# Performance work log

Hardware: AMD Instinct MI355X
Metric: run time of the kernel (lower is better)

Reference implementation:

```python
import jax, jax.numpy as jnp
import numpy as np

N_NODES = 100000
N_EDGES = 400000
IN_FEATS = 64
H_FEATS = 128
INTER = 128
NUM_CLASSES = 64


def setup_inputs() -> dict:
    key = jax.random.key(0)
    ks = jax.random.split(key, 32)
    inp = {}
    inp['gate_type'] = jax.random.randint(ks[0], (N_NODES,), 0, IN_FEATS)
    inp['src'] = jax.random.randint(ks[1], (N_EDGES,), 0, N_NODES)
    inp['dst'] = jax.random.randint(ks[2], (N_EDGES,), 0, N_NODES)
    inp['src_idx'] = jax.random.uniform(ks[3], (N_EDGES,), dtype=jnp.float32)
    inp['dst_idx'] = jax.random.uniform(ks[4], (N_EDGES,), dtype=jnp.float32)
    inp['rev'] = jax.random.uniform(ks[5], (N_EDGES,), dtype=jnp.float32)
    inp['emb'] = jax.random.normal(ks[6], (IN_FEATS, IN_FEATS), dtype=jnp.float32) * 0.05
    dims = [(IN_FEATS, H_FEATS), (H_FEATS, H_FEATS), (H_FEATS, H_FEATS), (H_FEATS, H_FEATS), (H_FEATS, NUM_CLASSES)]
    k = 7
    for i, (fi, fo) in enumerate(dims, 1):
        # xavier-normal-like scaling
        inp[f'w1_{i}'] = jax.random.normal(ks[k], (INTER, fi + 3), dtype=jnp.float32) * np.float32(np.sqrt(2.0 / (fi + 3 + INTER))); k += 1
        inp[f'w2_{i}'] = jax.random.normal(ks[k], (fo, fi + INTER), dtype=jnp.float32) * np.float32(np.sqrt(2.0 / (fi + INTER + fo))); k += 1
        inp[f'b2_{i}'] = jnp.zeros((fo,), dtype=jnp.float32); k += 1
    return inp


def _qconv(h, src, dst, w_edge, W1, W2, b2):
    # message: concat src node feats with edge feats -> [E, d+3]
    m = jnp.concatenate([h[src], w_edge], axis=1)
    # linear1 (no bias) + leaky_relu (torch default slope 0.01)
    tmp = jax.nn.leaky_relu(m @ W1.T, negative_slope=0.01)  # [E, inter]
    # mean-reduce per destination node (isolated nodes -> zeros, matching DGL)
    s = jax.ops.segment_sum(tmp, dst, num_segments=h.shape[0])
    cnt = jax.ops.segment_sum(jnp.ones((dst.shape[0],), tmp.dtype), dst, num_segments=h.shape[0])
    h_N = s / jnp.maximum(cnt, 1.0)[:, None]
    # linear2 on [h, h_N]
    return jnp.concatenate([h, h_N], axis=1) @ W2.T + b2


def reference(gate_type, src, dst, src_idx, dst_idx, rev, emb,
              w1_1, w2_1, b2_1, w1_2, w2_2, b2_2, w1_3, w2_3, b2_3,
              w1_4, w2_4, b2_4, w1_5, w2_5, b2_5):
    h = emb[gate_type]  # [N, in_feats]
    w_edge = jnp.stack([src_idx, dst_idx, rev], axis=1)  # [E, 3]
    layers = [(w1_1, w2_1, b2_1), (w1_2, w2_2, b2_2), (w1_3, w2_3, b2_3),
              (w1_4, w2_4, b2_4), (w1_5, w2_5, b2_5)]
    for i, (W1, W2, b2) in enumerate(layers):
        h = _qconv(h, src, dst, w_edge, W1, W2, b2)
        if i < 4:
            h = jax.nn.relu(h)
    return h
```

## Files before the change

### kernel.cpp

```cpp
#include <hip/hip_runtime.h>
#include <hip/hip_fp16.h>

typedef __attribute__((ext_vector_type(8))) short short8;
typedef __attribute__((ext_vector_type(4))) float f32x4;
typedef unsigned short u16;

__device__ __forceinline__ u16 f2bf(float f) {
    unsigned u = __float_as_uint(f);
    unsigned r = ((u >> 16) & 1) + 0x7FFFu;
    return (u16)((u + r) >> 16);
}

__device__ __forceinline__ unsigned pk_fma(unsigned a, unsigned b, unsigned c) {
    unsigned d;
    asm("v_pk_fma_f16 %0, %1, %2, %3" : "=v"(d) : "v"(a), "v"(b), "v"(c));
    return d;
}
__device__ __forceinline__ unsigned pk_mul(unsigned a, unsigned b) {
    unsigned d;
    asm("v_pk_mul_f16 %0, %1, %2" : "=v"(d) : "v"(a), "v"(b));
    return d;
}
__device__ __forceinline__ unsigned pk_max(unsigned a, unsigned b) {
    unsigned d;
    asm("v_pk_max_f16 %0, %1, %2" : "=v"(d) : "v"(a), "v"(b));
    return d;
}


__global__ void k_count(const int* __restrict__ dst, int* __restrict__ cnt, int E) {
    int i = blockIdx.x * 256 + threadIdx.x;
    if (i < E) atomicAdd(&cnt[dst[i]], 1);
}

__global__ void k_scan1(const int* __restrict__ cnt, int* __restrict__ partial, int N) {
    __shared__ int sm[256];
    int idx = blockIdx.x * 256 + threadIdx.x;
    sm[threadIdx.x] = (idx < N) ? cnt[idx] : 0;
    __syncthreads();
    for (int s = 128; s > 0; s >>= 1) {
        if (threadIdx.x < s) sm[threadIdx.x] += sm[threadIdx.x + s];
        __syncthreads();
    }
    if (threadIdx.x == 0) partial[blockIdx.x] = sm[0];
}

__global__ void k_scan2(int* __restrict__ partial, int nb) {
    __shared__ int sm[512];
    int t = threadIdx.x;
    sm[t] = (t < nb) ? partial[t] : 0;
    __syncthreads();
    for (int off = 1; off < 512; off <<= 1) {
        int v = (t >= off) ? sm[t - off] : 0;
        __syncthreads();
        sm[t] += v;
        __syncthreads();
    }
    if (t < nb) partial[t] = (t == 0) ? 0 : sm[t - 1];
}

__global__ void k_scan3(const int* __restrict__ cnt, const int* __restrict__ partial,
                        int* __restrict__ row_off, int* __restrict__ cursor,
                        float* __restrict__ invdeg, int N, int E) {
    __shared__ int sm[256];
    int idx = blockIdx.x * 256 + threadIdx.x;
    int v = (idx < N) ? cnt[idx] : 0;
    sm[threadIdx.x] = v;
    __syncthreads();
    for (int off = 1; off < 256; off <<= 1) {
        int u = (threadIdx.x >= off) ? sm[threadIdx.x - off] : 0;
        __syncthreads();
        sm[threadIdx.x] += u;
        __syncthreads();
    }
    if (idx < N) {
        int excl = partial[blockIdx.x] + sm[threadIdx.x] - v;
        row_off[idx] = excl;
        cursor[idx] = excl;
        invdeg[idx] = 1.0f / (float)((v > 1) ? v : 1);
    }
    if (idx == 0) row_off[N] = E;
}

__global__ void k_scatter(const int* __restrict__ dst, const int* __restrict__ src,
                          const float* __restrict__ sidx, const float* __restrict__ didx,
                          const float* __restrict__ rev,
                          int* __restrict__ cursor, int4* __restrict__ payload, int E) {
    int i = blockIdx.x * 256 + threadIdx.x;
    if (i < E) {
        int p = atomicAdd(&cursor[dst[i]], 1);
        unsigned hs = (unsigned)__half_as_ushort(__float2half_rn(sidx[i]));
        unsigned hd = (unsigned)__half_as_ushort(__float2half_rn(didx[i]));
        unsigned hr = (unsigned)__half_as_ushort(__float2half_rn(rev[i]));
        int4 v;
        v.x = src[i];
        v.y = (int)(hs * 0x10001u);
        v.z = (int)(hd * 0x10001u);
        v.w = (int)(hr * 0x10001u);
        payload[p] = v;
    }
}


__global__ void k_emb(const int* __restrict__ gt, const float* __restrict__ emb,
                      u16* __restrict__ h0, int N) {
    int i = blockIdx.x * 256 + threadIdx.x;
    if (i < N * 64) {
        int n = i >> 6, f = i & 63;
        h0[i] = f2bf(emb[(gt[n] << 6) | f]);
    }
}


struct WDesc {
    const float* src[10];
    u16* dst[10];
    int scols[10];
    int dcols[10];
    int n[10];
};

__global__ void k_wconv(WDesc d) {
    int seg = blockIdx.y;
    int idx = blockIdx.x * 256 + threadIdx.x;
    if (idx < d.n[seg]) {
        int dc = d.dcols[seg];
        int r = idx / dc, c = idx % dc;
        d.dst[seg][idx] = f2bf(d.src[seg][r * d.scols[seg] + c]);
    }
}

struct EDesc {
    const float* src[5];
    unsigned* dst[5];
    int ldw[5];
    int fi[5];
};

__global__ void k_wedge(EDesc d) {
    int l = blockIdx.x;
    int i = threadIdx.x;
    if (i < 192) {
        int c = i >> 6, j = i & 63;
        float a = d.src[l][(size_t)(2 * j) * d.ldw[l] + d.fi[l] + c];
        float b = d.src[l][(size_t)(2 * j + 1) * d.ldw[l] + d.fi[l] + c];
        unsigned lo = (unsigned)__half_as_ushort(__float2half_rn(a));
        unsigned hi = (unsigned)__half_as_ushort(__float2half_rn(b));
        d.dst[l][(c << 6) + j] = lo | (hi << 16);
    }
}


__global__ __launch_bounds__(256)
void k_edge(int N,
            const int* __restrict__ row_off, const int4* __restrict__ payload,
            const u16* __restrict__ g,
            const unsigned* __restrict__ W1h,
            const float* __restrict__ invdeg,
            u16* __restrict__ hN)
{
    const int t = threadIdx.x;
    const int lane = t & 63;
    const int fl = lane & 15;
    const int eg = lane >> 4;
    const int wid = blockIdx.x * (blockDim.x >> 6) + (t >> 6);
    const int nwtot = gridDim.x * (blockDim.x >> 6);
    const int per = (N + nwtot - 1) / nwtot;
    const int n0 = wid * per;
    if (n0 >= N) return;
    const int n1 = (n0 + per < N) ? (n0 + per) : N;

    const uint4 wa = *(const uint4*)&W1h[(fl << 2)];
    const uint4 wb = *(const uint4*)&W1h[64 + (fl << 2)];
    const uint4 wc = *(const uint4*)&W1h[128 + (fl << 2)];
    const unsigned c001 = ((unsigned)__half_as_ushort(__float2half_rn(0.01f))) * 0x10001u;

    int beg = row_off[n0];
    for (int n = n0; n < n1; ++n) {
        const int end = row_off[n + 1];
        float acc[8] = {0.f, 0.f, 0.f, 0.f, 0.f, 0.f, 0.f, 0.f};

        int p = beg + eg;
        int4 pl;
        if (p < end) pl = payload[p];
        while (p < end) {
            const int pn = p + 4;
            int4 plN = pl;
            if (pn < end) plN = payload[pn];
            const uint4 gv = *(const uint4*)(g + ((size_t)pl.x << 7) + (fl << 3));
            const unsigned si = (unsigned)pl.y;
            const unsigned di = (unsigned)pl.z;
            const unsigned rv = (unsigned)pl.w;
            unsigned v0 = pk_fma(wa.x, si, gv.x);
            unsigned v1 = pk_fma(wa.y, si, gv.y);
            unsigned v2 = pk_fma(wa.z, si, gv.z);
            unsigned v3 = pk_fma(wa.w, si, gv.w);
            v0 = pk_fma(wb.x, di, v0);
            v1 = pk_fma(wb.y, di, v1);
            v2 = pk_fma(wb.z, di, v2);
            v3 = pk_fma(wb.w, di, v3);
            v0 = pk_fma(wc.x, rv, v0);
            v1 = pk_fma(wc.y, rv, v1);
            v2 = pk_fma(wc.z, rv, v2);
            v3 = pk_fma(wc.w, rv, v3);
            v0 = pk_max(v0, pk_mul(v0, c001));
            v1 = pk_max(v1, pk_mul(v1, c001));
            v2 = pk_max(v2, pk_mul(v2, c001));
            v3 = pk_max(v3, pk_mul(v3, c001));
            const float2 f0 = __half22float2(*(const __half2*)&v0);
            const float2 f1 = __half22float2(*(const __half2*)&v1);
            const float2 f2 = __half22float2(*(const __half2*)&v2);
            const float2 f3 = __half22float2(*(const __half2*)&v3);
            acc[0] += f0.x; acc[1] += f0.y;
            acc[2] += f1.x; acc[3] += f1.y;
            acc[4] += f2.x; acc[5] += f2.y;
            acc[6] += f3.x; acc[7] += f3.y;
            p = pn;
            pl = plN;
        }

#pragma unroll
        for (int r = 0; r < 8; r++) {
            acc[r] += __shfl_xor(acc[r], 16, 64);
            acc[r] += __shfl_xor(acc[r], 32, 64);
        }

        if (eg == 0) {
            const float inv = invdeg[n];
            unsigned q0 = (unsigned)f2bf(acc[0] * inv) | ((unsigned)f2bf(acc[1] * inv) << 16);
            unsigned q1 = (unsigned)f2bf(acc[2] * inv) | ((unsigned)f2bf(acc[3] * inv) << 16);
            unsigned q2 = (unsigned)f2bf(acc[4] * inv) | ((unsigned)f2bf(acc[5] * inv) << 16);
            unsigned q3 = (unsigned)f2bf(acc[6] * inv) | ((unsigned)f2bf(acc[7] * inv) << 16);
            uint4 out = make_uint4(q0, q1, q2, q3);
            *(uint4*)(hN + ((size_t)n << 7) + (fl << 3)) = out;
        }
        beg = end;
    }
}


template<int K, int O, int SPLIT, int BIAS, int RELU, int OUTDT, int FUSE>
__global__ __launch_bounds__(256, 4)
void k_gemm(int M,
            const u16* __restrict__ A1, int lda1,
            const u16* __restrict__ A2, int lda2,
            const u16* __restrict__ W,
            const float* __restrict__ bias,
            void* __restrict__ Cout, int ldc,
            const u16* __restrict__ Wg,
            u16* __restrict__ Gout)
{
    constexpr int NF = O / 32;
    constexpr int WC = O / 2;
    __shared__ __align__(16) char Hbuf[FUSE ? 128 * 256 : 16];

    const int t = threadIdx.x;
    const int m0 = blockIdx.x * 128;
    const int w = t >> 6, l = t & 63;
    const int wm = w & 1, wn = w >> 1;
    const int lr = l & 15, lh = l >> 4;

    int arow[4];
#pragma unroll
    for (int mi = 0; mi < 4; mi++) {
        int m = m0 + wm * 64 + mi * 16 + lr;
        arow[mi] = (m < M) ? m : (M - 1);
    }

    f32x4 acc[4][NF];
#pragma unroll
    for (int mi = 0; mi < 4; mi++)
#pragma unroll
        for (int ni = 0; ni < NF; ni++) acc[mi][ni] = (f32x4){0.f, 0.f, 0.f, 0.f};

#pragma unroll
    for (int kt = 0; kt < K / 32; ++kt) {
        const int k0 = kt * 32;
        const u16* Abase;
        int lda, kof;
        if (k0 < SPLIT) { Abase = A1; lda = lda1; kof = k0; }
        else            { Abase = A2; lda = lda2; kof = k0 - SPLIT; }
        short8 a[4], b[NF];
#pragma unroll
        for (int mi = 0; mi < 4; mi++)
            a[mi] = *(const short8*)(Abase + (size_t)arow[mi] * lda + kof + lh * 8);
#pragma unroll
        for (int ni = 0; ni < NF; ni++)
            b[ni] = *(const short8*)(W + (size_t)(wn * WC + ni * 16 + lr) * K + k0 + lh * 8);
#pragma unroll
        for (int mi = 0; mi < 4; mi++)
#pragma unroll
            for (int ni = 0; ni < NF; ni++)
                acc[mi][ni] = __builtin_amdgcn_mfma_f32_16x16x32_bf16(a[mi], b[ni], acc[mi][ni], 0, 0, 0);
    }

    float bv[NF];
#pragma unroll
    for (int ni = 0; ni < NF; ni++)
        bv[ni] = BIAS ? bias[wn * WC + ni * 16 + lr] : 0.f;
#pragma unroll
    for (int mi = 0; mi < 4; mi++) {
#pragma unroll
        for (int i = 0; i < 4; i++) {
            int rloc = wm * 64 + mi * 16 + lh * 4 + i;
            int row = m0 + rloc;
#pragma unroll
            for (int ni = 0; ni < NF; ni++) {
                float v = acc[mi][ni][i] + bv[ni];
                if (RELU) v = fmaxf(v, 0.f);
                int col = wn * WC + ni * 16 + lr;
                if (FUSE) {
                    u16 hv = f2bf(v);
                    *(u16*)(Hbuf + rloc * 256 + ((col * 2) ^ ((rloc & 15) << 4))) = hv;
                    if (row < M) ((u16*)Cout)[(size_t)row * ldc + col] = hv;
                } else if (row < M) {
                    if (OUTDT == 1)      ((u16*)Cout)[(size_t)row * ldc + col] = f2bf(v);
                    else if (OUTDT == 2) ((__half*)Cout)[(size_t)row * ldc + col] = __float2half(v);
                    else                 ((float*)Cout)[(size_t)row * ldc + col] = v;
                }
            }
        }
    }

    if (FUSE) {
        __syncthreads();
        f32x4 acc2[4][4];
#pragma unroll
        for (int mi = 0; mi < 4; mi++)
#pragma unroll
            for (int ni = 0; ni < 4; ni++) acc2[mi][ni] = (f32x4){0.f, 0.f, 0.f, 0.f};

#pragma unroll
        for (int kt = 0; kt < 4; ++kt) {
            const int k0 = kt * 32;
            short8 a[4], b[4];
#pragma unroll
            for (int mi = 0; mi < 4; mi++) {
                int r = wm * 64 + mi * 16 + lr;
                a[mi] = *(const short8*)(Hbuf + r * 256 + (((k0 + lh * 8) * 2) ^ ((r & 15) << 4)));
            }
#pragma unroll
            for (int ni = 0; ni < 4; ni++)
                b[ni] = *(const short8*)(Wg + (size_t)(wn * 64 + ni * 16 + lr) * 128 + k0 + lh * 8);
#pragma unroll
            for (int mi = 0; mi < 4; mi++)
#pragma unroll
                for (int ni = 0; ni < 4; ni++)
                    acc2[mi][ni] = __builtin_amdgcn_mfma_f32_16x16x32_bf16(a[mi], b[ni], acc2[mi][ni], 0, 0, 0);
        }

#pragma unroll
        for (int mi = 0; mi < 4; mi++) {
#pragma unroll
            for (int i = 0; i < 4; i++) {
                int row = m0 + wm * 64 + mi * 16 + lh * 4 + i;
                if (row < M) {
#pragma unroll
                    for (int ni = 0; ni < 4; ni++) {
                        int col = wn * 64 + ni * 16 + lr;
                        ((__half*)Gout)[(size_t)row * 128 + col] = __float2half(acc2[mi][ni][i]);
                    }
                }
            }
        }
    }
}


extern "C" void kernel_launch(void* const* d_in, const int* in_sizes, int n_in,
                              void* d_out, int out_size, void* d_ws, size_t ws_size,
                              hipStream_t stream)
{
    const int N = in_sizes[0];
    const int E = in_sizes[1];
    const int* gate = (const int*)d_in[0];
    const int* src = (const int*)d_in[1];
    const int* dst = (const int*)d_in[2];
    const float* sidx = (const float*)d_in[3];
    const float* didx = (const float*)d_in[4];
    const float* rev = (const float*)d_in[5];
    const float* emb = (const float*)d_in[6];
    const float* w1[5] = {(const float*)d_in[7], (const float*)d_in[10], (const float*)d_in[13],
                          (const float*)d_in[16], (const float*)d_in[19]};
    const float* w2[5] = {(const float*)d_in[8], (const float*)d_in[11], (const float*)d_in[14],
                          (const float*)d_in[17], (const float*)d_in[20]};
    const float* b2[5] = {(const float*)d_in[9], (const float*)d_in[12], (const float*)d_in[15],
                          (const float*)d_in[18], (const float*)d_in[21]};

    char* ws = (char*)d_ws;
    size_t off = 0;
    auto alloc = [&](size_t bytes) {
        void* p = ws + off;
        off = (off + bytes + 255) & ~(size_t)255;
        return p;
    };
    u16* hb0 = (u16*)alloc((size_t)N * 128 * 2);
    u16* hb1 = (u16*)alloc((size_t)N * 128 * 2);
    u16* hN = (u16*)alloc((size_t)N * 128 * 2);
    u16* g = (u16*)alloc((size_t)N * 128 * 2);
    int* cnt = (int*)alloc((size_t)N * 4);
    int* row_off = (int*)alloc((size_t)(N + 1) * 4);
    int* cursor = (int*)alloc((size_t)N * 4);
    int4* payload = (int4*)alloc((size_t)E * 16);
    int* partial = (int*)alloc(512 * 4);
    float* invd = (float*)alloc((size_t)N * 4);
    unsigned* w1h = (unsigned*)alloc(5 * 192 * 4);
    u16* w1b[5];
    u16* w2b[5];
    const int fis[5] = {64, 128, 128, 128, 128};
    for (int i = 0; i < 5; i++) w1b[i] = (u16*)alloc((size_t)128 * fis[i] * 2);
    for (int i = 0; i < 5; i++) {
        int fo = (i == 4) ? 64 : 128;
        w2b[i] = (u16*)alloc((size_t)fo * (fis[i] + 128) * 2);
    }

    WDesc wd;
    for (int i = 0; i < 5; i++) {
        wd.src[i] = w1[i]; wd.dst[i] = w1b[i];
        wd.scols[i] = fis[i] + 3; wd.dcols[i] = fis[i]; wd.n[i] = 128 * fis[i];
        int fo = (i == 4) ? 64 : 128;
        wd.src[5 + i] = w2[i]; wd.dst[5 + i] = w2b[i];
        wd.scols[5 + i] = fis[i] + 128; wd.dcols[5 + i] = fis[i] + 128;
        wd.n[5 + i] = fo * (fis[i] + 128);
    }
    k_wconv<<<dim3(128, 10), dim3(256), 0, stream>>>(wd);

    EDesc ed;
    for (int i = 0; i < 5; i++) {
        ed.src[i] = w1[i];
        ed.dst[i] = w1h + i * 192;
        ed.ldw[i] = fis[i] + 3;
        ed.fi[i] = fis[i];
    }
    k_wedge<<<dim3(5), dim3(192), 0, stream>>>(ed);

    hipMemsetAsync(cnt, 0, (size_t)N * 4, stream);
    k_count<<<dim3((E + 255) / 256), dim3(256), 0, stream>>>(dst, cnt, E);
    const int nb = (N + 255) / 256;
    k_scan1<<<dim3(nb), dim3(256), 0, stream>>>(cnt, partial, N);
    k_scan2<<<dim3(1), dim3(512), 0, stream>>>(partial, nb);
    k_scan3<<<dim3(nb), dim3(256), 0, stream>>>(cnt, partial, row_off, cursor, invd, N, E);
    k_scatter<<<dim3((E + 255) / 256), dim3(256), 0, stream>>>(dst, src, sidx, didx, rev, cursor, payload, E);
    k_emb<<<dim3((N * 64 + 255) / 256), dim3(256), 0, stream>>>(gate, emb, hb0, N);

    const int gg = (N + 127) / 128;
    const int eb = 2048;

    k_gemm<64, 128, 64, 0, 0, 2, 0><<<dim3(gg), dim3(256), 0, stream>>>(
        N, hb0, 64, (const u16*)nullptr, 0, w1b[0], (const float*)nullptr, g, 128,
        (const u16*)nullptr, (u16*)nullptr);
    k_edge<<<dim3(eb), dim3(256), 0, stream>>>(N, row_off, payload, g, w1h + 0 * 192, invd, hN);
    k_gemm<192, 128, 64, 1, 1, 1, 1><<<dim3(gg), dim3(256), 0, stream>>>(
        N, hb0, 64, hN, 128, w2b[0], b2[0], hb1, 128, w1b[1], g);

    u16* hcur = hb1;
    u16* hnxt = hb0;
    for (int l = 1; l < 4; ++l) {
        k_edge<<<dim3(eb), dim3(256), 0, stream>>>(N, row_off, payload, g, w1h + l * 192, invd, hN);
        k_gemm<256, 128, 128, 1, 1, 1, 1><<<dim3(gg), dim3(256), 0, stream>>>(
            N, hcur, 128, hN, 128, w2b[l], b2[l], hnxt, 128, w1b[l + 1], g);
        u16* tmp = hcur; hcur = hnxt; hnxt = tmp;
    }

    k_edge<<<dim3(eb), dim3(256), 0, stream>>>(N, row_off, payload, g, w1h + 4 * 192, invd, hN);
    k_gemm<256, 64, 128, 1, 0, 0, 0><<<dim3(gg), dim3(256), 0, stream>>>(
        N, hcur, 128, hN, 128, w2b[4], b2[4], (float*)d_out, 64,
        (const u16*)nullptr, (u16*)nullptr);
}
```

Measured before the change: 476.7 us.

## Stage GEMM weights and A tiles in LDS with 512-thread blocks

The node GEMM kernel now copies the whole weight matrix into padded shared memory once per block. It also stages each 128x32 activation tile into shared memory through direct global-to-LDS loads, and moves from 4 to 8 waves per block. The fused second GEMM now reads the freshly written H back from global memory instead of a swizzled LDS buffer, and reuses the weight LDS region for Wg. The aim is to remove redundant global reads of W by every wave. The cost is an extra barrier pair per K step, larger LDS use that may reduce occupancy, and a global round trip for H.

```diff
diff --git a/kernel.cpp b/kernel.cpp
--- a/kernel.cpp
+++ b/kernel.cpp
@@ -9,6 +9,12 @@
     unsigned u = __float_as_uint(f);
     unsigned r = ((u >> 16) & 1) + 0x7FFFu;
     return (u16)((u + r) >> 16);
+}
+
+__device__ __forceinline__ void gload_lds16(const void* g, void* l) {
+    __builtin_amdgcn_global_load_lds((const __attribute__((address_space(1))) unsigned int*)g,
+                                     (__attribute__((address_space(3))) unsigned int*)l,
+                                     16, 0, 0);
 }
 
 __device__ __forceinline__ unsigned pk_fma(unsigned a, unsigned b, unsigned c) {
@@ -240,7 +246,7 @@
 
 
 template<int K, int O, int SPLIT, int BIAS, int RELU, int OUTDT, int FUSE>
-__global__ __launch_bounds__(256, 4)
+__global__ __launch_bounds__(512, 4)
 void k_gemm(int M,
             const u16* __restrict__ A1, int lda1,
             const u16* __restrict__ A2, int lda2,
@@ -250,48 +256,69 @@
             const u16* __restrict__ Wg,
             u16* __restrict__ Gout)
 {
+    constexpr int KP = K + 8;
+    constexpr int HP = 136;
     constexpr int NF = O / 32;
     constexpr int WC = O / 2;
-    __shared__ __align__(16) char Hbuf[FUSE ? 128 * 256 : 16];
+    __shared__ __align__(16) u16 Wlds[O * KP];
+    __shared__ __align__(16) u16 Atile[128 * 32];
 
     const int t = threadIdx.x;
     const int m0 = blockIdx.x * 128;
     const int w = t >> 6, l = t & 63;
-    const int wm = w & 1, wn = w >> 1;
+    const int wm = w & 3, wn = w >> 2;
     const int lr = l & 15, lh = l >> 4;
 
-    int arow[4];
-#pragma unroll
-    for (int mi = 0; mi < 4; mi++) {
-        int m = m0 + wm * 64 + mi * 16 + lr;
-        arow[mi] = (m < M) ? m : (M - 1);
-    }
-
-    f32x4 acc[4][NF];
-#pragma unroll
-    for (int mi = 0; mi < 4; mi++)
+    for (int idx = t; idx < O * (K / 8); idx += 512) {
+        int row = idx / (K / 8), ch = idx % (K / 8);
+        uint4 v = *(const uint4*)(W + (size_t)row * K + ch * 8);
+        *(uint4*)(&Wlds[row * KP + ch * 8]) = v;
+    }
+
+    f32x4 acc[2][NF];
+#pragma unroll
+    for (int mi = 0; mi < 2; mi++)
 #pragma unroll
         for (int ni = 0; ni < NF; ni++) acc[mi][ni] = (f32x4){0.f, 0.f, 0.f, 0.f};
 
-#pragma unroll
+    __syncthreads();
+
     for (int kt = 0; kt < K / 32; ++kt) {
         const int k0 = kt * 32;
-        const u16* Abase;
+        const u16* Asrc;
         int lda, kof;
-        if (k0 < SPLIT) { Abase = A1; lda = lda1; kof = k0; }
-        else            { Abase = A2; lda = lda2; kof = k0 - SPLIT; }
-        short8 a[4], b[NF];
-#pragma unroll
-        for (int mi = 0; mi < 4; mi++)
-            a[mi] = *(const short8*)(Abase + (size_t)arow[mi] * lda + kof + lh * 8);
+        if (k0 < SPLIT) { Asrc = A1; lda = lda1; kof = k0; }
+        else            { Asrc = A2; lda = lda2; kof = k0 - SPLIT; }
+        {
+            int o = t * 16;
+            int row = o >> 6;
+            int m = m0 + row;
+            m = (m < M) ? m : (M - 1);
+            gload_lds16(Asrc + (size_t)m * lda + kof + ((t & 3) << 3), (void*)(Atile + (o >> 1)));
+        }
+        __syncthreads();
+
+        short8 a[2], b[NF];
+#pragma unroll
+        for (int mi = 0; mi < 2; mi++)
+            a[mi] = *(const short8*)(Atile + (wm * 32 + mi * 16 + lr) * 32 + lh * 8);
 #pragma unroll
         for (int ni = 0; ni < NF; ni++)
-            b[ni] = *(const short8*)(W + (size_t)(wn * WC + ni * 16 + lr) * K + k0 + lh * 8);
-#pragma unroll
-        for (int mi = 0; mi < 4; mi++)
+            b[ni] = *(const short8*)(Wlds + (size_t)(wn * WC + ni * 16 + lr) * KP + k0 + lh * 8);
+#pragma unroll
+        for (int mi = 0; mi < 2; mi++)
 #pragma unroll
             for (int ni = 0; ni < NF; ni++)
                 acc[mi][ni] = __builtin_amdgcn_mfma_f32_16x16x32_bf16(a[mi], b[ni], acc[mi][ni], 0, 0, 0);
+        __syncthreads();
+    }
+
+    if (FUSE) {
+        for (int idx = t; idx < 128 * 16; idx += 512) {
+            int row = idx >> 4, ch = idx & 15;
+            uint4 v = *(const uint4*)(Wg + (size_t)row * 128 + ch * 8);
+            *(uint4*)(&Wlds[row * HP + ch * 8]) = v;
+        }
     }
 
     float bv[NF];
@@ -299,24 +326,19 @@
     for (int ni = 0; ni < NF; ni++)
         bv[ni] = BIAS ? bias[wn * WC + ni * 16 + lr] : 0.f;
 #pragma unroll
-    for (int mi = 0; mi < 4; mi++) {
+    for (int mi = 0; mi < 2; mi++) {
 #pragma unroll
         for (int i = 0; i < 4; i++) {
-            int rloc = wm * 64 + mi * 16 + lh * 4 + i;
-            int row = m0 + rloc;
-#pragma unroll
-            for (int ni = 0; ni < NF; ni++) {
-                float v = acc[mi][ni][i] + bv[ni];
-                if (RELU) v = fmaxf(v, 0.f);
-                int col = wn * WC + ni * 16 + lr;
-                if (FUSE) {
-                    u16 hv = f2bf(v);
-                    *(u16*)(Hbuf + rloc * 256 + ((col * 2) ^ ((rloc & 15) << 4))) = hv;
-                    if (row < M) ((u16*)Cout)[(size_t)row * ldc + col] = hv;
-                } else if (row < M) {
-                    if (OUTDT == 1)      ((u16*)Cout)[(size_t)row * ldc + col] = f2bf(v);
-                    else if (OUTDT == 2) ((__half*)Cout)[(size_t)row * ldc + col] = __float2half(v);
-                    else                 ((float*)Cout)[(size_t)row * ldc + col] = v;
+            int row = m0 + wm * 32 + mi * 16 + lh * 4 + i;
+            if (row < M) {
+#pragma unroll
+                for (int ni = 0; ni < NF; ni++) {
+                    float v = acc[mi][ni][i] + bv[ni];
+                    if (RELU) v = fmaxf(v, 0.f);
+                    int col = wn * WC + ni * 16 + lr;
+                    if (FUSE || OUTDT == 1) ((u16*)Cout)[(size_t)row * ldc + col] = f2bf(v);
+                    else if (OUTDT == 2)    ((__half*)Cout)[(size_t)row * ldc + col] = __float2half(v);
+                    else                    ((float*)Cout)[(size_t)row * ldc + col] = v;
                 }
             }
         }
@@ -324,36 +346,43 @@
 
     if (FUSE) {
         __syncthreads();
-        f32x4 acc2[4][4];
-#pragma unroll
-        for (int mi = 0; mi < 4; mi++)
+
+        const u16* H = (const u16*)Cout;
+        int hrow[2];
+#pragma unroll
+        for (int mi = 0; mi < 2; mi++) {
+            int m = m0 + wm * 32 + mi * 16 + lr;
+            hrow[mi] = (m < M) ? m : (M - 1);
+        }
+
+        f32x4 acc2[2][4];
+#pragma unroll
+        for (int mi = 0; mi < 2; mi++)
 #pragma unroll
             for (int ni = 0; ni < 4; ni++) acc2[mi][ni] = (f32x4){0.f, 0.f, 0.f, 0.f};
 
 #pragma unroll
         for (int kt = 0; kt < 4; ++kt) {
             const int k0 = kt * 32;
-            short8 a[4], b[4];
-#pragma unroll
-            for (int mi = 0; mi < 4; mi++) {
-                int r = wm * 64 + mi * 16 + lr;
-                a[mi] = *(const short8*)(Hbuf + r * 256 + (((k0 + lh * 8) * 2) ^ ((r & 15) << 4)));
-            }
+            short8 a[2], b[4];
+#pragma unroll
+            for (int mi = 0; mi < 2; mi++)
+                a[mi] = *(const short8*)(H + (size_t)hrow[mi] * ldc + k0 + lh * 8);
 #pragma unroll
             for (int ni = 0; ni < 4; ni++)
-                b[ni] = *(const short8*)(Wg + (size_t)(wn * 64 + ni * 16 + lr) * 128 + k0 + lh * 8);
-#pragma unroll
-            for (int mi = 0; mi < 4; mi++)
+                b[ni] = *(const short8*)(Wlds + (size_t)(wn * 64 + ni * 16 + lr) * HP + k0 + lh * 8);
+#pragma unroll
+            for (int mi = 0; mi < 2; mi++)
 #pragma unroll
                 for (int ni = 0; ni < 4; ni++)
                     acc2[mi][ni] = __builtin_amdgcn_mfma_f32_16x16x32_bf16(a[mi], b[ni], acc2[mi][ni], 0, 0, 0);
         }
 
 #pragma unroll
-        for (int mi = 0; mi < 4; mi++) {
+        for (int mi = 0; mi < 2; mi++) {
 #pragma unroll
             for (int i = 0; i < 4; i++) {
-                int row = m0 + wm * 64 + mi * 16 + lh * 4 + i;
+                int row = m0 + wm * 32 + mi * 16 + lh * 4 + i;
                 if (row < M) {
 #pragma unroll
                     for (int ni = 0; ni < 4; ni++) {
@@ -446,24 +475,24 @@
     const int gg = (N + 127) / 128;
     const int eb = 2048;
 
-    k_gemm<64, 128, 64, 0, 0, 2, 0><<<dim3(gg), dim3(256), 0, stream>>>(
+    k_gemm<64, 128, 64, 0, 0, 2, 0><<<dim3(gg), dim3(512), 0, stream>>>(
         N, hb0, 64, (const u16*)nullptr, 0, w1b[0], (const float*)nullptr, g, 128,
         (const u16*)nullptr, (u16*)nullptr);
     k_edge<<<dim3(eb), dim3(256), 0, stream>>>(N, row_off, payload, g, w1h + 0 * 192, invd, hN);
-    k_gemm<192, 128, 64, 1, 1, 1, 1><<<dim3(gg), dim3(256), 0, stream>>>(
+    k_gemm<192, 128, 64, 1, 1, 1, 1><<<dim3(gg), dim3(512), 0, stream>>>(
         N, hb0, 64, hN, 128, w2b[0], b2[0], hb1, 128, w1b[1], g);
 
     u16* hcur = hb1;
     u16* hnxt = hb0;
     for (int l = 1; l < 4; ++l) {
         k_edge<<<dim3(eb), dim3(256), 0, stream>>>(N, row_off, payload, g, w1h + l * 192, invd, hN);
-        k_gemm<256, 128, 128, 1, 1, 1, 1><<<dim3(gg), dim3(256), 0, stream>>>(
+        k_gemm<256, 128, 128, 1, 1, 1, 1><<<dim3(gg), dim3(512), 0, stream>>>(
             N, hcur, 128, hN, 128, w2b[l], b2[l], hnxt, 128, w1b[l + 1], g);
         u16* tmp = hcur; hcur = hnxt; hnxt = tmp;
     }
 
     k_edge<<<dim3(eb), dim3(256), 0, stream>>>(N, row_off, payload, g, w1h + 4 * 192, invd, hN);
-    k_gemm<256, 64, 128, 1, 0, 0, 0><<<dim3(gg), dim3(256), 0, stream>>>(
+    k_gemm<256, 64, 128, 1, 0, 0, 0><<<dim3(gg), dim3(512), 0, stream>>>(
         N, hcur, 128, hN, 128, w2b[4], b2[4], (float*)d_out, 64,
         (const u16*)nullptr, (u16*)nullptr);
 }
```

Result: faster. 413.1 us (-13.4%).
